# Kernel optimization log

Hardware: AMD Instinct MI355X
Metric: run time of the kernel (lower is better)

## Reference

```python
import jax, jax.numpy as jnp
import numpy as np

B, DIN, DL, DOUT = 8192, 512, 512, 512
L, H, DFF = 6, 8, 2048
E, K = 8, 2
HID = 1024  # int(dim_latent * 2.0)
SLOPE = 0.01
EPS = 1e-5


def _ln(x, s, b):
    m = x.mean(-1, keepdims=True)
    v = ((x - m) ** 2).mean(-1, keepdims=True)
    return (x - m) / jnp.sqrt(v + EPS) * s + b


def _lrelu(x):
    return jnp.where(x >= 0, x, SLOPE * x)


def _mha(q_in, kv_in, in_w, in_b, out_w, out_b):
    # torch nn.MultiheadAttention math (batch_first). in_w: [3d, d]
    d = q_in.shape[-1]
    hd = d // H
    wq, wk, wv = jnp.split(in_w, 3, axis=0)
    bq, bk, bv = jnp.split(in_b, 3, axis=0)
    q = (q_in @ wq.T + bq).reshape(q_in.shape[0], -1, H, hd)
    k = (kv_in @ wk.T + bk).reshape(kv_in.shape[0], -1, H, hd)
    v = (kv_in @ wv.T + bv).reshape(kv_in.shape[0], -1, H, hd)
    scale = jnp.asarray(hd, q.dtype) ** 0.5
    att = jax.nn.softmax(jnp.einsum('bqhd,bkhd->bhqk', q, k) / scale, axis=-1)
    o = jnp.einsum('bhqk,bkhd->bqhd', att, v).reshape(q_in.shape[0], -1, d)
    return o @ out_w.T + out_b


def setup_inputs() -> dict:
    key = jax.random.key(0)
    ks = iter(jax.random.split(key, 64))
    def n(shape, scale=0.02):
        return jax.random.normal(next(ks), shape, dtype=jnp.float32) * scale
    inp = dict(
        src=jax.random.normal(next(ks), (B, 2, DIN), dtype=jnp.float32),
        piw=n((DL, DIN)), pib=n((DL,)), pos=n((1, 2, DL), 1.0),
        ln1_s=jnp.ones((L, DL)), ln1_b=jnp.zeros((L, DL)),
        ln2_s=jnp.ones((L, DL)), ln2_b=jnp.zeros((L, DL)),
        ln3_s=jnp.ones((L, DL)), ln3_b=jnp.zeros((L, DL)),
        sa_in_w=n((L, 3 * DL, DL)), sa_in_b=n((L, 3 * DL)),
        sa_out_w=n((L, DL, DL)), sa_out_b=n((L, DL)),
        ca_in_w=n((L, 3 * DL, DL)), ca_in_b=n((L, 3 * DL)),
        ca_out_w=n((L, DL, DL)), ca_out_b=n((L, DL)),
        ff1_w=n((L, DFF, DL)), ff1_b=n((L, DFF)),
        ff2_w=n((L, DL, DFF)), ff2_b=n((L, DL)),
        r1_w=n((DL // 2, DL)), r1_b=n((DL // 2,)),
        r2_w=n((E, DL // 2)), r2_b=n((E,)),
        se1_w=n((HID, DL)), se1_b=n((HID,)),
        se2_w=n((HID // 2, HID)), se2_b=n((HID // 2,)),
        se3_w=n((DOUT, HID // 2)), se3_b=n((DOUT,)),
        te1_w=n((E, HID, DL)), te1_b=n((E, HID)),
        te2_w=n((E, HID // 2, HID)), te2_b=n((E, HID // 2)),
        te3_w=n((E, DOUT, HID // 2)), te3_b=n((E, DOUT)),
        po_w=n((DOUT, DOUT * (E + 1))), po_b=n((DOUT,)),
    )
    return inp


def reference(src, piw, pib, pos,
              ln1_s, ln1_b, ln2_s, ln2_b, ln3_s, ln3_b,
              sa_in_w, sa_in_b, sa_out_w, sa_out_b,
              ca_in_w, ca_in_b, ca_out_w, ca_out_b,
              ff1_w, ff1_b, ff2_w, ff2_b,
              r1_w, r1_b, r2_w, r2_b,
              se1_w, se1_b, se2_w, se2_b, se3_w, se3_b,
              te1_w, te1_b, te2_w, te2_b, te3_w, te3_b,
              po_w, po_b):
    # input projection + positional encoding; split into tgt (pos 0) / mem (pos 1)
    x = src @ piw.T + pib + pos              # [B, 2, DL]
    tgt, mem = x[:, 0:1], x[:, 1:2]
    # norm_first TransformerDecoderLayer stack (eval: no dropout)
    for i in range(L):
        h = _ln(tgt, ln1_s[i], ln1_b[i])
        tgt = tgt + _mha(h, h, sa_in_w[i], sa_in_b[i], sa_out_w[i], sa_out_b[i])
        h = _ln(tgt, ln2_s[i], ln2_b[i])
        tgt = tgt + _mha(h, mem, ca_in_w[i], ca_in_b[i], ca_out_w[i], ca_out_b[i])
        h = _ln(tgt, ln3_s[i], ln3_b[i])
        tgt = tgt + jax.nn.relu(h @ ff1_w[i].T + ff1_b[i]) @ ff2_w[i].T + ff2_b[i]
    t = tgt[:, 0]                             # [B, DL]
    # shared expert MLP
    sh = _lrelu(t @ se1_w.T + se1_b)
    sh = _lrelu(sh @ se2_w.T + se2_b)
    sh = sh @ se3_w.T + se3_b                 # [B, DOUT]
    # top-k gating (sparse softmax over top-k logits)
    logits = _lrelu(t @ r1_w.T + r1_b) @ r2_w.T + r2_b   # [B, E]
    top_vals, top_idx = jax.lax.top_k(logits, K)
    probs = jax.nn.softmax(top_vals, axis=-1)
    gates = jnp.zeros_like(logits).at[jnp.arange(t.shape[0])[:, None], top_idx].set(probs)
    # dense all-experts compute; non-selected experts get gate=0, which is
    # mathematically identical to the torch mask/gather/scatter dispatch
    h1 = _lrelu(jnp.einsum('bd,ehd->beh', t, te1_w) + te1_b)     # [B,E,HID]
    h2 = _lrelu(jnp.einsum('beh,egh->beg', h1, te2_w) + te2_b)   # [B,E,HID//2]
    eo = jnp.einsum('beg,eog->beo', h2, te3_w) + te3_b           # [B,E,DOUT]
    weighted = (eo * gates[..., None]).reshape(t.shape[0], E * DOUT)
    out = jnp.concatenate([sh, weighted], axis=-1) @ po_w.T + po_b
    return out
```

## Files before the change

### kernel.cpp

```cpp
#include <hip/hip_runtime.h>
#include <hip/hip_bf16.h>

typedef __attribute__((ext_vector_type(8))) short bf8_t;
typedef __attribute__((ext_vector_type(4))) float f4_t;

#define DEV static __device__ __forceinline__

DEV short f2bf(float x){
  unsigned u = __float_as_uint(x);
  u += 0x7fffu + ((u >> 16) & 1u);
  return (short)(u >> 16);
}
DEV float bf2f(short h){
  return __uint_as_float(((unsigned)(unsigned short)h) << 16);
}

DEV void swz(int& bx, int& by){
  int gx = gridDim.x, n = gx * gridDim.y;
  int lb = blockIdx.x + gx * blockIdx.y;
  int q = n >> 3, r = n & 7, xcd = lb & 7, idx = lb >> 3;
  int s = (xcd < r) ? (xcd * (q + 1) + idx) : (r * (q + 1) + (xcd - r) * q + idx);
  bx = s % gx; by = s / gx;
}

template<int TM, int TN, bool SPLIT, int ACT, int MODE, int LB>
__global__ __launch_bounds__(256, LB)
void g2_k(const short* __restrict__ Ahi, const short* __restrict__ Alo, int lda,
          const short* __restrict__ Whi, const short* __restrict__ Wlo, int ldw, long wzs,
          const float* __restrict__ bias, long bzs,
          const float* __restrict__ res, int ldres,
          const float* __restrict__ scale,
          float* __restrict__ Df, int ldd,
          short* __restrict__ Dhi, short* __restrict__ Dlo, int lddp,
          const int* __restrict__ off, const int* __restrict__ perm, int K)
{
  constexpr int NS = SPLIT ? 2 : 1;
  constexpr int TM2 = TM / 2, TN2 = TN / 2, AM = TM / 32, AN = TN / 32;
  constexpr int AIT = TM / 64, BIT = TN / 64;
  __shared__ short As[NS][TM][40];
  __shared__ short Bs[NS][TN][40];

  int bx, by; swz(bx, by);
  const int rowStart = by * TM, colStart = bx * TN;
  if constexpr (MODE >= 1) {
    if (rowStart >= off[8]) return;
    int e = 0;
    while (rowStart >= off[e + 1]) ++e;
    Whi += (long)e * wzs;
    if constexpr (SPLIT) Wlo += (long)e * wzs;
    bias += (long)e * bzs;
  }

  const int tid = threadIdx.x, lane = tid & 63, wid = tid >> 6;
  const int wr = wid >> 1, wc = wid & 1, fr = lane & 15, kg = lane >> 4;

  f4_t acc[AM][AN];
#pragma unroll
  for (int m = 0; m < AM; m++)
#pragma unroll
    for (int n = 0; n < AN; n++)
#pragma unroll
      for (int j = 0; j < 4; j++) acc[m][n][j] = 0.f;

  const short* pAh[AIT]; const short* pAl[AIT]; int aLr[AIT], aLc[AIT];
#pragma unroll
  for (int it = 0; it < AIT; it++) {
    int idx = tid + it * 256, r = idx >> 2, c8 = (idx & 3) << 3;
    aLr[it] = r; aLc[it] = c8;
    long rg = rowStart + r;
    if constexpr (MODE == 2) { int p = perm[rg]; rg = p < 0 ? 0 : p; }
    pAh[it] = Ahi + rg * (long)lda + c8;
    if constexpr (SPLIT) pAl[it] = Alo + rg * (long)lda + c8;
  }
  const short* pBh[BIT]; const short* pBl[BIT]; int bLr[BIT], bLc[BIT];
#pragma unroll
  for (int it = 0; it < BIT; it++) {
    int idx = tid + it * 256, r = idx >> 2, c8 = (idx & 3) << 3;
    bLr[it] = r; bLc[it] = c8;
    long rg = colStart + r;
    pBh[it] = Whi + rg * (long)ldw + c8;
    if constexpr (SPLIT) pBl[it] = Wlo + rg * (long)ldw + c8;
  }

  for (int kb = 0; kb < K; kb += 32) {
    bf8_t va[AIT], val[AIT], vb[BIT], vbl[BIT];
#pragma unroll
    for (int it = 0; it < AIT; it++) {
      va[it] = *(const bf8_t*)(pAh[it] + kb);
      if constexpr (SPLIT) val[it] = *(const bf8_t*)(pAl[it] + kb);
    }
#pragma unroll
    for (int it = 0; it < BIT; it++) {
      vb[it] = *(const bf8_t*)(pBh[it] + kb);
      if constexpr (SPLIT) vbl[it] = *(const bf8_t*)(pBl[it] + kb);
    }
    __syncthreads();
#pragma unroll
    for (int it = 0; it < AIT; it++) {
      *(bf8_t*)&As[0][aLr[it]][aLc[it]] = va[it];
      if constexpr (SPLIT) *(bf8_t*)&As[1][aLr[it]][aLc[it]] = val[it];
    }
#pragma unroll
    for (int it = 0; it < BIT; it++) {
      *(bf8_t*)&Bs[0][bLr[it]][bLc[it]] = vb[it];
      if constexpr (SPLIT) *(bf8_t*)&Bs[1][bLr[it]][bLc[it]] = vbl[it];
    }
    __syncthreads();

    bf8_t a0[AM], a1[AM], b0[AN], b1[AN];
#pragma unroll
    for (int m = 0; m < AM; m++) {
      a0[m] = *(const bf8_t*)&As[0][wr * TM2 + m * 16 + fr][kg * 8];
      if constexpr (SPLIT) a1[m] = *(const bf8_t*)&As[1][wr * TM2 + m * 16 + fr][kg * 8];
    }
#pragma unroll
    for (int n = 0; n < AN; n++) {
      b0[n] = *(const bf8_t*)&Bs[0][wc * TN2 + n * 16 + fr][kg * 8];
      if constexpr (SPLIT) b1[n] = *(const bf8_t*)&Bs[1][wc * TN2 + n * 16 + fr][kg * 8];
    }
#pragma unroll
    for (int m = 0; m < AM; m++)
#pragma unroll
      for (int n = 0; n < AN; n++) {
        acc[m][n] = __builtin_amdgcn_mfma_f32_16x16x32_bf16(a0[m], b0[n], acc[m][n], 0, 0, 0);
        if constexpr (SPLIT) {
          acc[m][n] = __builtin_amdgcn_mfma_f32_16x16x32_bf16(a0[m], b1[n], acc[m][n], 0, 0, 0);
          acc[m][n] = __builtin_amdgcn_mfma_f32_16x16x32_bf16(a1[m], b0[n], acc[m][n], 0, 0, 0);
        }
      }
  }

#pragma unroll
  for (int m = 0; m < AM; m++) {
#pragma unroll
    for (int n = 0; n < AN; n++) {
      const int col = colStart + wc * TN2 + n * 16 + fr;
#pragma unroll
      for (int j = 0; j < 4; j++) {
        const int row = rowStart + wr * TM2 + m * 16 + kg * 4 + j;
        float v = acc[m][n][j];
        if (bias) v += bias[col];
        if (ACT == 1) v = fmaxf(v, 0.f);
        if (ACT == 2) v = (v >= 0.f) ? v : 0.01f * v;
        if (scale) v *= scale[row];
        if (res) v += res[(size_t)row * ldres + col];
        if (Df) Df[(size_t)row * ldd + col] = v;
        if (Dhi) {
          short h = f2bf(v);
          Dhi[(size_t)row * lddp + col] = h;
          if (Dlo) Dlo[(size_t)row * lddp + col] = f2bf(v - bf2f(h));
        }
      }
    }
  }
}

template<bool SPLIT, bool DEMUX>
__global__ __launch_bounds__(256, 2)
void g1_k(const float* __restrict__ A, int lda, long zsA,
          const float* __restrict__ W, int ldw, long zsB,
          const float* __restrict__ bias, int posbias,
          float* __restrict__ Df, short* __restrict__ Dhi, short* __restrict__ Dlo,
          int ldd, long zsD, int K)
{
  constexpr int NS = SPLIT ? 2 : 1;
  __shared__ short As[NS][128][40];
  __shared__ short Bs[NS][128][40];
  const long z = blockIdx.z;
  A += z * zsA; W += z * zsB;
  if (Df)  Df  += z * zsD;
  if (Dhi) Dhi += z * zsD;

  int bx, by; swz(bx, by);
  const int tid = threadIdx.x, lane = tid & 63, wid = tid >> 6;
  const int wr = wid >> 1, wc = wid & 1, fr = lane & 15, kg = lane >> 4;

  f4_t acc[4][4];
#pragma unroll
  for (int m = 0; m < 4; m++)
#pragma unroll
    for (int n = 0; n < 4; n++)
#pragma unroll
      for (int j = 0; j < 4; j++) acc[m][n][j] = 0.f;

  const int srow = tid >> 1, skoff = (tid & 1) << 4;
  const float* pA = A + (size_t)((size_t)by * 128 + srow) * lda + skoff;
  const float* pW = W + (size_t)((size_t)bx * 128 + srow) * ldw + skoff;

  for (int kb = 0; kb < K; kb += 32) {
    float va[16], vw[16];
    {
      const f4_t* a4 = (const f4_t*)(pA + kb);
      const f4_t* w4 = (const f4_t*)(pW + kb);
#pragma unroll
      for (int q = 0; q < 4; q++) {
        f4_t ta = a4[q], tw = w4[q];
#pragma unroll
        for (int j = 0; j < 4; j++) { va[q * 4 + j] = ta[j]; vw[q * 4 + j] = tw[j]; }
      }
    }
    __syncthreads();
#pragma unroll
    for (int h = 0; h < 2; h++) {
      bf8_t ha, hw;
#pragma unroll
      for (int j = 0; j < 8; j++) { ha[j] = f2bf(va[h * 8 + j]); hw[j] = f2bf(vw[h * 8 + j]); }
      *(bf8_t*)&As[0][srow][skoff + h * 8] = ha;
      *(bf8_t*)&Bs[0][srow][skoff + h * 8] = hw;
      if constexpr (SPLIT) {
        bf8_t la, lw;
#pragma unroll
        for (int j = 0; j < 8; j++) {
          la[j] = f2bf(va[h * 8 + j] - bf2f(ha[j]));
          lw[j] = f2bf(vw[h * 8 + j] - bf2f(hw[j]));
        }
        *(bf8_t*)&As[NS - 1][srow][skoff + h * 8] = la;
        *(bf8_t*)&Bs[NS - 1][srow][skoff + h * 8] = lw;
      }
    }
    __syncthreads();

    bf8_t a0[4], b0[4], a1[4], b1[4];
#pragma unroll
    for (int m = 0; m < 4; m++) {
      a0[m] = *(const bf8_t*)&As[0][wr * 64 + m * 16 + fr][kg * 8];
      if constexpr (SPLIT) a1[m] = *(const bf8_t*)&As[NS - 1][wr * 64 + m * 16 + fr][kg * 8];
    }
#pragma unroll
    for (int n = 0; n < 4; n++) {
      b0[n] = *(const bf8_t*)&Bs[0][wc * 64 + n * 16 + fr][kg * 8];
      if constexpr (SPLIT) b1[n] = *(const bf8_t*)&Bs[NS - 1][wc * 64 + n * 16 + fr][kg * 8];
    }
#pragma unroll
    for (int m = 0; m < 4; m++)
#pragma unroll
      for (int n = 0; n < 4; n++) {
        acc[m][n] = __builtin_amdgcn_mfma_f32_16x16x32_bf16(a0[m], b0[n], acc[m][n], 0, 0, 0);
        if constexpr (SPLIT) {
          acc[m][n] = __builtin_amdgcn_mfma_f32_16x16x32_bf16(a0[m], b1[n], acc[m][n], 0, 0, 0);
          acc[m][n] = __builtin_amdgcn_mfma_f32_16x16x32_bf16(a1[m], b0[n], acc[m][n], 0, 0, 0);
        }
      }
  }

  const int Ncols = (int)gridDim.x * 128;
#pragma unroll
  for (int m = 0; m < 4; m++) {
#pragma unroll
    for (int n = 0; n < 4; n++) {
      const int col = bx * 128 + wc * 64 + n * 16 + fr;
#pragma unroll
      for (int j = 0; j < 4; j++) {
        const int row = by * 128 + wr * 64 + m * 16 + kg * 4 + j;
        float v = acc[m][n][j];
        if (bias) v += bias[posbias ? ((row & 1) * Ncols + col) : col];
        if constexpr (DEMUX) {
          const size_t o = (size_t)(row >> 1) * ldd + col;
          if (row & 1) { short h = f2bf(v); Dhi[o] = h; Dlo[o] = f2bf(v - bf2f(h)); }
          else Df[o] = v;
        } else {
          if (Dhi) Dhi[(size_t)row * ldd + col] = f2bf(v);
          else     Df[(size_t)row * ldd + col] = v;
        }
      }
    }
  }
}

__global__ __launch_bounds__(256)
void ln2_k(const float* __restrict__ x, int ldx,
           const float* __restrict__ s, const float* __restrict__ b,
           short* __restrict__ hi, short* __restrict__ lo, int ldy)
{
  const int lane = threadIdx.x & 63;
  const int row = blockIdx.x * 4 + (threadIdx.x >> 6);
  const float* xr = x + (size_t)row * ldx + lane * 8;
  f4_t v0 = *(const f4_t*)xr;
  f4_t v1 = *(const f4_t*)(xr + 4);
  float sum = (v0[0] + v0[1]) + (v0[2] + v0[3]) + ((v1[0] + v1[1]) + (v1[2] + v1[3]));
#pragma unroll
  for (int o = 32; o; o >>= 1) sum += __shfl_xor(sum, o, 64);
  const float mean = sum * (1.f / 512.f);
  float vs = 0.f;
#pragma unroll
  for (int j = 0; j < 4; j++) { float d0 = v0[j] - mean, d1 = v1[j] - mean; vs += d0 * d0 + d1 * d1; }
#pragma unroll
  for (int o = 32; o; o >>= 1) vs += __shfl_xor(vs, o, 64);
  const float rstd = rsqrtf(vs * (1.f / 512.f) + 1e-5f);
  const float* sp = s + lane * 8; const float* bp = b + lane * 8;
  bf8_t h, l;
#pragma unroll
  for (int j = 0; j < 4; j++) {
    float y0 = (v0[j] - mean) * rstd * sp[j] + bp[j];
    float y1 = (v1[j] - mean) * rstd * sp[j + 4] + bp[j + 4];
    short h0 = f2bf(y0); h[j] = h0;     l[j] = f2bf(y0 - bf2f(h0));
    short h1 = f2bf(y1); h[j + 4] = h1; l[j + 4] = f2bf(y1 - bf2f(h1));
  }
  *(bf8_t*)&hi[(size_t)row * ldy + lane * 8] = h;
  *(bf8_t*)&lo[(size_t)row * ldy + lane * 8] = l;
}

__global__ __launch_bounds__(256)
void conv_k(const float* __restrict__ src, long zs, int ld, int cols,
            short* __restrict__ hi, short* __restrict__ lo, long dzs)
{
  const long z = blockIdx.z;
  int idx = blockIdx.x * 256 + threadIdx.x;
  int cpr = cols >> 3;
  int row = idx / cpr, c8 = (idx % cpr) << 3;
  const float* p = src + z * zs + (size_t)row * ld + c8;
  f4_t v0 = *(const f4_t*)p, v1 = *(const f4_t*)(p + 4);
  bf8_t h, l;
#pragma unroll
  for (int j = 0; j < 4; j++) {
    short h0 = f2bf(v0[j]); h[j] = h0;     l[j] = f2bf(v0[j] - bf2f(h0));
    short h1 = f2bf(v1[j]); h[j + 4] = h1; l[j + 4] = f2bf(v1[j] - bf2f(h1));
  }
  size_t dof = (size_t)z * dzs + (size_t)row * cols + c8;
  *(bf8_t*)&hi[dof] = h;
  if (lo) *(bf8_t*)&lo[dof] = l;
}

__global__ __launch_bounds__(256)
void tr_k(const float* __restrict__ in, float* __restrict__ out)
{
  __shared__ float t[32][33];
  const int e = blockIdx.z, ob = blockIdx.x * 32, gb = blockIdx.y * 32;
  const int tx = threadIdx.x & 31, ty = threadIdx.x >> 5;
  const float* I = in + ((size_t)e * 512 + ob) * 512 + gb;
  float* O = out + ((size_t)e * 512 + gb) * 512 + ob;
#pragma unroll
  for (int i = 0; i < 4; i++) t[ty + 8 * i][tx] = I[(size_t)(ty + 8 * i) * 512 + tx];
  __syncthreads();
#pragma unroll
  for (int i = 0; i < 4; i++) O[(size_t)(ty + 8 * i) * 512 + tx] = t[tx][ty + 8 * i];
}

__global__ __launch_bounds__(256)
void bc_k(const float* __restrict__ po, const float* __restrict__ te3b, float* __restrict__ bc)
{
  int idx = blockIdx.x * 256 + threadIdx.x;
  int e = idx >> 9, oo = idx & 511;
  const float* p = po + (size_t)oo * 4608 + 512 + (size_t)e * 512;
  const float* tb = te3b + (size_t)e * 512;
  float s = 0.f;
#pragma unroll 4
  for (int g = 0; g < 512; g += 4) {
    f4_t a = *(const f4_t*)(p + g);
    f4_t b = *(const f4_t*)(tb + g);
    s += a[0] * b[0] + a[1] * b[1] + a[2] * b[2] + a[3] * b[3];
  }
  bc[idx] = s;
}

__global__ __launch_bounds__(256)
void init_k(int* __restrict__ cnt, int* __restrict__ perm, float* __restrict__ pgate)
{
  int i = blockIdx.x * 256 + threadIdx.x;
  if (i < 16) cnt[i] = 0;
  if (i < 17408) { perm[i] = -1; pgate[i] = 0.f; }
}

__global__ __launch_bounds__(256)
void router_k(const float* __restrict__ R1, const float* __restrict__ r2w,
              const float* __restrict__ r2b, int2* __restrict__ ridx,
              float2* __restrict__ rgv, int* __restrict__ cnt)
{
  const int lane = threadIdx.x & 63;
  const int row = blockIdx.x * 4 + (threadIdx.x >> 6);
  f4_t xv = *(const f4_t*)(R1 + (size_t)row * 256 + lane * 4);
  float lg[8];
#pragma unroll
  for (int e = 0; e < 8; e++) {
    f4_t wv = *(const f4_t*)(r2w + e * 256 + lane * 4);
    float p = xv[0] * wv[0] + xv[1] * wv[1] + xv[2] * wv[2] + xv[3] * wv[3];
#pragma unroll
    for (int o = 32; o; o >>= 1) p += __shfl_xor(p, o, 64);
    lg[e] = p + r2b[e];
  }
  int i1 = 0; float v1 = lg[0];
#pragma unroll
  for (int e = 1; e < 8; e++) if (lg[e] > v1) { v1 = lg[e]; i1 = e; }
  int i2 = -1; float v2 = -3.4e38f;
#pragma unroll
  for (int e = 0; e < 8; e++) if (e != i1 && lg[e] > v2) { v2 = lg[e]; i2 = e; }
  const float p2 = 1.f / (1.f + expf(v1 - v2));
  const float p1 = 1.f - p2;
  if (lane == 0) {
    ridx[row] = make_int2(i1, i2);
    rgv[row] = make_float2(p1, p2);
    atomicAdd(&cnt[i1], 1); atomicAdd(&cnt[i2], 1);
  }
}

__global__ void offs_k(const int* __restrict__ cnt, int* __restrict__ off)
{
  if (threadIdx.x == 0) {
    int a = 0; off[0] = 0;
    for (int e = 0; e < 8; e++) { a += (cnt[e] + 127) & ~127; off[e + 1] = a; }
  }
}

__global__ __launch_bounds__(256)
void scat_k(const int2* __restrict__ ridx, const float2* __restrict__ rgv,
            const int* __restrict__ off, int* __restrict__ fill,
            int* __restrict__ perm, float* __restrict__ pgate, int2* __restrict__ islot)
{
  int r = blockIdx.x * 256 + threadIdx.x;
  int2 ii = ridx[r]; float2 gg = rgv[r];
  int p0 = off[ii.x] + atomicAdd(&fill[ii.x], 1); perm[p0] = r; pgate[p0] = gg.x;
  int p1 = off[ii.y] + atomicAdd(&fill[ii.y], 1); perm[p1] = r; pgate[p1] = gg.y;
  islot[r] = make_int2(p0, p1);
}

__global__ __launch_bounds__(256)
void fadd_k(const int2* __restrict__ islot, const float* __restrict__ EO, float* __restrict__ out)
{
  int idx = blockIdx.x * 256 + threadIdx.x;
  int r = idx >> 7, c4 = (idx & 127) << 2;
  int2 s = islot[r];
  f4_t a = *(const f4_t*)&EO[(size_t)s.x * 512 + c4];
  f4_t b = *(const f4_t*)&EO[(size_t)s.y * 512 + c4];
  float* op = &out[(size_t)r * 512 + c4];
  f4_t o = *(const f4_t*)op;
#pragma unroll
  for (int j = 0; j < 4; j++) o[j] += a[j] + b[j];
  *(f4_t*)op = o;
}

__global__ void bias2_k(const float* __restrict__ pib, const float* __restrict__ pos,
                        float* __restrict__ bias2)
{
  int i = blockIdx.x * 256 + threadIdx.x;
  if (i < 1024) bias2[i] = pib[i & 511] + pos[i];
}


extern "C" void kernel_launch(void* const* d_in, const int* in_sizes, int n_in,
                              void* d_out, int out_size, void* d_ws, size_t ws_size,
                              hipStream_t stream)
{
  (void)in_sizes; (void)n_in; (void)out_size; (void)ws_size;
  const float* src     = (const float*)d_in[0];
  const float* piw     = (const float*)d_in[1];
  const float* pib     = (const float*)d_in[2];
  const float* pos     = (const float*)d_in[3];
  const float* ln1_s   = (const float*)d_in[4];
  const float* ln1_b   = (const float*)d_in[5];
  const float* ln3_s   = (const float*)d_in[8];
  const float* ln3_b   = (const float*)d_in[9];
  const float* sa_in_w = (const float*)d_in[10];
  const float* sa_in_b = (const float*)d_in[11];
  const float* sa_ow   = (const float*)d_in[12];
  const float* sa_ob   = (const float*)d_in[13];
  const float* ca_in_w = (const float*)d_in[14];
  const float* ca_in_b = (const float*)d_in[15];
  const float* ca_ow   = (const float*)d_in[16];
  const float* ca_ob   = (const float*)d_in[17];
  const float* ff1_w   = (const float*)d_in[18];
  const float* ff1_b   = (const float*)d_in[19];
  const float* ff2_w   = (const float*)d_in[20];
  const float* ff2_b   = (const float*)d_in[21];
  const float* r1_w    = (const float*)d_in[22];
  const float* r1_b    = (const float*)d_in[23];
  const float* r2_w    = (const float*)d_in[24];
  const float* r2_b    = (const float*)d_in[25];
  const float* se1_w   = (const float*)d_in[26];
  const float* se1_b   = (const float*)d_in[27];
  const float* se2_w   = (const float*)d_in[28];
  const float* se2_b   = (const float*)d_in[29];
  const float* se3_w   = (const float*)d_in[30];
  const float* se3_b   = (const float*)d_in[31];
  const float* te1_w   = (const float*)d_in[32];
  const float* te1_b   = (const float*)d_in[33];
  const float* te2_w   = (const float*)d_in[34];
  const float* te2_b   = (const float*)d_in[35];
  const float* te3_w   = (const float*)d_in[36];
  const float* te3_b   = (const float*)d_in[37];
  const float* po_w    = (const float*)d_in[38];
  const float* po_b    = (const float*)d_in[39];
  float* out = (float*)d_out;

  const size_t MiB = 1048576;
  char* base = (char*)d_ws;
  float* tgt   = (float*)(base + 0 * MiB);
  short* MemHi = (short*)(base + 16 * MiB);
  short* MemLo = (short*)(base + 24 * MiB);
  short* Hhi   = (short*)(base + 32 * MiB);
  short* Hlo   = (short*)(base + 40 * MiB);
  short* Fhi   = (short*)(base + 48 * MiB);
  short* Flo   = (short*)(base + 80 * MiB);
  short* Vhi   = (short*)(base + 48 * MiB);
  short* Vlo   = (short*)(base + 56 * MiB);
  short* wsV   = (short*)(base + 112 * MiB);
  short* saVhi = wsV;             short* saVlo = wsV + 262144;
  short* saOhi = wsV + 524288;    short* saOlo = wsV + 786432;
  short* caVhi = wsV + 1048576;   short* caVlo = wsV + 1310720;
  short* caOhi = wsV + 1572864;   short* caOlo = wsV + 1835008;
  short* ff1hi = (short*)(base + 116 * MiB);  short* ff1lo = ff1hi + 1048576;
  short* ff2hi = (short*)(base + 120 * MiB);  short* ff2lo = ff2hi + 1048576;
  short* tgtHi = Hhi;  short* tgtLo = Hlo;
  float* te3T  = (float*)(base + 0 * MiB);
  short* S1hi  = (short*)(base + 0 * MiB);
  short* S2hi  = (short*)(base + 16 * MiB);
  short* SHhi  = (short*)(base + 24 * MiB);
  short* X1hi  = (short*)(base + 48 * MiB);
  short* X2hi  = (short*)(base + 82 * MiB);
  float* EO    = (float*)(base + 48 * MiB);
  float* F2    = (float*)(base + 104 * MiB);
  short* te1hi = (short*)(base + 104 * MiB);
  short* te2hi = (short*)(base + 112 * MiB);
  short* Wchi  = (short*)(base + 120 * MiB);
  char*  ps    = base + 124 * MiB;
  size_t cur = 0;
  auto alloc = [&](size_t bytes) { char* r = ps + cur; cur = (cur + bytes + 255) & ~(size_t)255; return r; };
  float*  bias2 = (float*)alloc(1024 * 4);
  float*  bc    = (float*)alloc(4096 * 4);
  int*    cnt   = (int*)  alloc(64 * 4);
  int*    fill  = cnt + 8;
  int*    offs  = cnt + 16;
  int2*   ridx  = (int2*) alloc(8192 * 8);
  float2* rgv   = (float2*)alloc(8192 * 8);
  int2*   islot = (int2*) alloc(8192 * 8);
  int*    perm  = (int*)  alloc(17408 * 4);
  float*  pgate = (float*)alloc(17408 * 4);
  short*  r1hi  = (short*)alloc(524288);  short* r1lo = r1hi + 131072;
  short*  se1hi = (short*)alloc(1048576);
  short*  se2hi = (short*)alloc(1048576);
  short*  se3hi = (short*)alloc(524288);
  short*  pomhi = (short*)alloc(524288);

  auto conv = [&](const float* s_, long zs, int ld, int rows, int cols, int z,
                  short* hi, short* lo, long dzs) {
    conv_k<<<dim3(rows * cols / 2048, 1, z), dim3(256), 0, stream>>>(s_, zs, ld, cols, hi, lo, dzs);
  };

  bias2_k<<<dim3(4), dim3(256), 0, stream>>>(pib, pos, bias2);
  conv(r1_w, 0, 512, 256, 512, 1, r1hi, r1lo, 0);
  conv(se1_w, 0, 512, 1024, 512, 1, se1hi, nullptr, 0);
  conv(se2_w, 0, 1024, 512, 1024, 1, se2hi, nullptr, 0);
  conv(se3_w, 0, 512, 512, 512, 1, se3hi, nullptr, 0);
  conv(po_w, 0, 4608, 512, 512, 1, pomhi, nullptr, 0);
  bc_k<<<dim3(16), dim3(256), 0, stream>>>(po_w, te3_b, bc);

  g1_k<true, true><<<dim3(4, 128, 1), dim3(256), 0, stream>>>(
      src, 512, 0, piw, 512, 0, bias2, 1, tgt, MemHi, MemLo, 512, 0, 512);

  for (int i = 0; i < 6; i++) {
    conv(sa_in_w + (size_t)i * 786432 + 524288, 0, 512, 512, 512, 1, saVhi, saVlo, 0);
    conv(sa_ow + (size_t)i * 262144, 0, 512, 512, 512, 1, saOhi, saOlo, 0);
    conv(ca_in_w + (size_t)i * 786432 + 524288, 0, 512, 512, 512, 1, caVhi, caVlo, 0);
    conv(ca_ow + (size_t)i * 262144, 0, 512, 512, 512, 1, caOhi, caOlo, 0);
    conv(ff1_w + (size_t)i * 1048576, 0, 512, 2048, 512, 1, ff1hi, ff1lo, 0);
    conv(ff2_w + (size_t)i * 1048576, 0, 2048, 512, 2048, 1, ff2hi, ff2lo, 0);

    ln2_k<<<dim3(2048), dim3(256), 0, stream>>>(tgt, 512, ln1_s + i * 512, ln1_b + i * 512, Hhi, Hlo, 512);
    g2_k<64, 128, true, 0, 0, 2><<<dim3(4, 128), 256, 0, stream>>>(
        Hhi, Hlo, 512, saVhi, saVlo, 512, 0, sa_in_b + i * 1536 + 1024, 0,
        nullptr, 0, nullptr, nullptr, 0, Vhi, Vlo, 512, nullptr, nullptr, 512);
    g2_k<64, 128, true, 0, 0, 2><<<dim3(4, 128), 256, 0, stream>>>(
        Vhi, Vlo, 512, saOhi, saOlo, 512, 0, sa_ob + i * 512, 0,
        tgt, 512, nullptr, tgt, 512, nullptr, nullptr, 0, nullptr, nullptr, 512);
    g2_k<64, 128, true, 0, 0, 2><<<dim3(4, 128), 256, 0, stream>>>(
        MemHi, MemLo, 512, caVhi, caVlo, 512, 0, ca_in_b + i * 1536 + 1024, 0,
        nullptr, 0, nullptr, nullptr, 0, Vhi, Vlo, 512, nullptr, nullptr, 512);
    g2_k<64, 128, true, 0, 0, 2><<<dim3(4, 128), 256, 0, stream>>>(
        Vhi, Vlo, 512, caOhi, caOlo, 512, 0, ca_ob + i * 512, 0,
        tgt, 512, nullptr, tgt, 512, nullptr, nullptr, 0, nullptr, nullptr, 512);
    ln2_k<<<dim3(2048), dim3(256), 0, stream>>>(tgt, 512, ln3_s + i * 512, ln3_b + i * 512, Hhi, Hlo, 512);
    g2_k<128, 128, true, 1, 0, 2><<<dim3(16, 64), 256, 0, stream>>>(
        Hhi, Hlo, 512, ff1hi, ff1lo, 512, 0, ff1_b + i * 2048, 0,
        nullptr, 0, nullptr, nullptr, 0, Fhi, Flo, 2048, nullptr, nullptr, 512);
    bool last = (i == 5);
    g2_k<64, 128, true, 0, 0, 2><<<dim3(4, 128), 256, 0, stream>>>(
        Fhi, Flo, 2048, ff2hi, ff2lo, 2048, 0, ff2_b + i * 512, 0,
        tgt, 512, nullptr, tgt, 512,
        last ? tgtHi : nullptr, last ? tgtLo : nullptr, 512, nullptr, nullptr, 2048);
  }

  init_k<<<dim3(68), dim3(256), 0, stream>>>(cnt, perm, pgate);
  g2_k<64, 128, true, 2, 0, 2><<<dim3(2, 128), 256, 0, stream>>>(
      tgtHi, tgtLo, 512, r1hi, r1lo, 512, 0, r1_b, 0,
      nullptr, 0, nullptr, F2, 256, nullptr, nullptr, 0, nullptr, nullptr, 512);
  router_k<<<dim3(2048), dim3(256), 0, stream>>>(F2, r2_w, r2_b, ridx, rgv, cnt);
  offs_k<<<dim3(1), dim3(64), 0, stream>>>(cnt, offs);
  scat_k<<<dim3(32), dim3(256), 0, stream>>>(ridx, rgv, offs, fill, perm, pgate, islot);

  tr_k<<<dim3(16, 16, 8), dim3(256), 0, stream>>>(te3_w, te3T);
  g1_k<false, false><<<dim3(4, 4, 8), dim3(256), 0, stream>>>(
      po_w + 512, 4608, 512, te3T, 512, 262144,
      nullptr, 0, nullptr, Wchi, nullptr, 512, 262144, 512);
  conv(te1_w, 524288, 512, 1024, 512, 8, te1hi, nullptr, 524288);
  conv(te2_w, 524288, 1024, 512, 1024, 8, te2hi, nullptr, 524288);

  g2_k<128, 128, false, 2, 0, 3><<<dim3(8, 64), 256, 0, stream>>>(
      tgtHi, nullptr, 512, se1hi, nullptr, 512, 0, se1_b, 0,
      nullptr, 0, nullptr, nullptr, 0, S1hi, nullptr, 1024, nullptr, nullptr, 512);
  g2_k<64, 128, false, 2, 0, 4><<<dim3(4, 128), 256, 0, stream>>>(
      S1hi, nullptr, 1024, se2hi, nullptr, 1024, 0, se2_b, 0,
      nullptr, 0, nullptr, nullptr, 0, S2hi, nullptr, 512, nullptr, nullptr, 1024);
  g2_k<64, 128, false, 0, 0, 4><<<dim3(4, 128), 256, 0, stream>>>(
      S2hi, nullptr, 512, se3hi, nullptr, 512, 0, se3_b, 0,
      nullptr, 0, nullptr, nullptr, 0, SHhi, nullptr, 512, nullptr, nullptr, 512);
  g2_k<64, 128, false, 0, 0, 4><<<dim3(4, 128), 256, 0, stream>>>(
      SHhi, nullptr, 512, pomhi, nullptr, 512, 0, po_b, 0,
      nullptr, 0, nullptr, out, 512, nullptr, nullptr, 0, nullptr, nullptr, 512);

  g2_k<128, 128, false, 2, 2, 3><<<dim3(8, 136), 256, 0, stream>>>(
      tgtHi, nullptr, 512, te1hi, nullptr, 512, 524288, te1_b, 1024,
      nullptr, 0, nullptr, nullptr, 0, X1hi, nullptr, 1024, offs, perm, 512);
  g2_k<64, 128, false, 2, 1, 4><<<dim3(4, 272), 256, 0, stream>>>(
      X1hi, nullptr, 1024, te2hi, nullptr, 1024, 524288, te2_b, 512,
      nullptr, 0, nullptr, nullptr, 0, X2hi, nullptr, 512, offs, nullptr, 1024);
  g2_k<64, 128, false, 0, 1, 4><<<dim3(4, 272), 256, 0, stream>>>(
      X2hi, nullptr, 512, Wchi, nullptr, 512, 262144, bc, 512,
      nullptr, 0, pgate, EO, 512, nullptr, nullptr, 0, offs, nullptr, 512);
  fadd_k<<<dim3(4096), dim3(256), 0, stream>>>(islot, EO, out);
}
```

Baseline: 2.822 ms.

## Fuse MoE dispatch into one ballot-based kernel and retune GEMM template parameter

Replaces the init, atomic-count, offset and atomic-scatter kernels with a single 1024-thread block. It counts experts per wave with ballots, builds the offsets in shared memory and assigns slots deterministically. This removes three launches and the global atomics. Separately, the last template parameter of most transformer-layer GEMMs changes from 2 to 4 (3 for ff1), which likely alters occupancy or pipelining depth. The single-block scheduler serialises 8192 rows on one CU, which adds some latency.

```diff
diff --git a/kernel.cpp b/kernel.cpp
--- a/kernel.cpp
+++ b/kernel.cpp
@@ -354,17 +354,9 @@
 }
 
 __global__ __launch_bounds__(256)
-void init_k(int* __restrict__ cnt, int* __restrict__ perm, float* __restrict__ pgate)
-{
-  int i = blockIdx.x * 256 + threadIdx.x;
-  if (i < 16) cnt[i] = 0;
-  if (i < 17408) { perm[i] = -1; pgate[i] = 0.f; }
-}
-
-__global__ __launch_bounds__(256)
 void router_k(const float* __restrict__ R1, const float* __restrict__ r2w,
               const float* __restrict__ r2b, int2* __restrict__ ridx,
-              float2* __restrict__ rgv, int* __restrict__ cnt)
+              float2* __restrict__ rgv)
 {
   const int lane = threadIdx.x & 63;
   const int row = blockIdx.x * 4 + (threadIdx.x >> 6);
@@ -389,28 +381,76 @@
   if (lane == 0) {
     ridx[row] = make_int2(i1, i2);
     rgv[row] = make_float2(p1, p2);
-    atomicAdd(&cnt[i1], 1); atomicAdd(&cnt[i2], 1);
-  }
-}
-
-__global__ void offs_k(const int* __restrict__ cnt, int* __restrict__ off)
-{
-  if (threadIdx.x == 0) {
-    int a = 0; off[0] = 0;
-    for (int e = 0; e < 8; e++) { a += (cnt[e] + 127) & ~127; off[e + 1] = a; }
-  }
-}
-
-__global__ __launch_bounds__(256)
-void scat_k(const int2* __restrict__ ridx, const float2* __restrict__ rgv,
-            const int* __restrict__ off, int* __restrict__ fill,
-            int* __restrict__ perm, float* __restrict__ pgate, int2* __restrict__ islot)
-{
-  int r = blockIdx.x * 256 + threadIdx.x;
-  int2 ii = ridx[r]; float2 gg = rgv[r];
-  int p0 = off[ii.x] + atomicAdd(&fill[ii.x], 1); perm[p0] = r; pgate[p0] = gg.x;
-  int p1 = off[ii.y] + atomicAdd(&fill[ii.y], 1); perm[p1] = r; pgate[p1] = gg.y;
-  islot[r] = make_int2(p0, p1);
+  }
+}
+
+__global__ __launch_bounds__(1024, 1)
+void sched_k(const int2* __restrict__ ridx, const float2* __restrict__ rgv,
+             int* __restrict__ offs, int* __restrict__ perm,
+             float* __restrict__ pgate, int2* __restrict__ islot)
+{
+  __shared__ int wcnt[16][8];
+  __shared__ int wbase[16][8];
+  __shared__ int soff[9];
+  const int tid = threadIdx.x, lane = tid & 63, w = tid >> 6;
+  const unsigned long long below = (lane == 63) ? 0x7FFFFFFFFFFFFFFFULL
+                                                : ((1ULL << lane) - 1);
+  int2 rid[8]; float2 rgl[8];
+  int cnt[8];
+#pragma unroll
+  for (int e = 0; e < 8; e++) cnt[e] = 0;
+#pragma unroll
+  for (int it = 0; it < 8; it++) {
+    int r = w * 512 + it * 64 + lane;
+    rid[it] = ridx[r]; rgl[it] = rgv[r];
+#pragma unroll
+    for (int e = 0; e < 8; e++) {
+      unsigned long long m0 = __ballot(rid[it].x == e);
+      unsigned long long m1 = __ballot(rid[it].y == e);
+      cnt[e] += (int)__popcll(m0) + (int)__popcll(m1);
+    }
+  }
+  if (lane == 0) {
+#pragma unroll
+    for (int e = 0; e < 8; e++) wcnt[w][e] = cnt[e];
+  }
+  __syncthreads();
+  if (tid == 0) {
+    int a = 0; soff[0] = 0;
+    for (int e = 0; e < 8; e++) {
+      int run = a, tot = 0;
+      for (int ww = 0; ww < 16; ww++) { wbase[ww][e] = run; run += wcnt[ww][e]; tot += wcnt[ww][e]; }
+      a += (tot + 127) & ~127;
+      soff[e + 1] = a;
+    }
+  }
+  __syncthreads();
+  if (tid < 9) offs[tid] = soff[tid];
+  for (int i = tid; i < 17408; i += 1024) { perm[i] = -1; pgate[i] = 0.f; }
+  __syncthreads();
+  int cur[8];
+#pragma unroll
+  for (int e = 0; e < 8; e++) cur[e] = wbase[w][e];
+#pragma unroll
+  for (int it = 0; it < 8; it++) {
+    int r = w * 512 + it * 64 + lane;
+    int p0 = 0, p1 = 0;
+#pragma unroll
+    for (int e = 0; e < 8; e++) {
+      unsigned long long m = __ballot(rid[it].x == e);
+      if (rid[it].x == e) p0 = cur[e] + (int)__popcll(m & below);
+      cur[e] += (int)__popcll(m);
+    }
+#pragma unroll
+    for (int e = 0; e < 8; e++) {
+      unsigned long long m = __ballot(rid[it].y == e);
+      if (rid[it].y == e) p1 = cur[e] + (int)__popcll(m & below);
+      cur[e] += (int)__popcll(m);
+    }
+    perm[p0] = r; pgate[p0] = rgl[it].x;
+    perm[p1] = r; pgate[p1] = rgl[it].y;
+    islot[r] = make_int2(p0, p1);
+  }
 }
 
 __global__ __launch_bounds__(256)
@@ -516,9 +556,7 @@
   auto alloc = [&](size_t bytes) { char* r = ps + cur; cur = (cur + bytes + 255) & ~(size_t)255; return r; };
   float*  bias2 = (float*)alloc(1024 * 4);
   float*  bc    = (float*)alloc(4096 * 4);
-  int*    cnt   = (int*)  alloc(64 * 4);
-  int*    fill  = cnt + 8;
-  int*    offs  = cnt + 16;
+  int*    offs  = (int*)  alloc(64 * 4);
   int2*   ridx  = (int2*) alloc(8192 * 8);
   float2* rgv   = (float2*)alloc(8192 * 8);
   int2*   islot = (int2*) alloc(8192 * 8);
@@ -555,36 +593,34 @@
     conv(ff2_w + (size_t)i * 1048576, 0, 2048, 512, 2048, 1, ff2hi, ff2lo, 0);
 
     ln2_k<<<dim3(2048), dim3(256), 0, stream>>>(tgt, 512, ln1_s + i * 512, ln1_b + i * 512, Hhi, Hlo, 512);
-    g2_k<64, 128, true, 0, 0, 2><<<dim3(4, 128), 256, 0, stream>>>(
+    g2_k<64, 128, true, 0, 0, 4><<<dim3(4, 128), 256, 0, stream>>>(
         Hhi, Hlo, 512, saVhi, saVlo, 512, 0, sa_in_b + i * 1536 + 1024, 0,
         nullptr, 0, nullptr, nullptr, 0, Vhi, Vlo, 512, nullptr, nullptr, 512);
-    g2_k<64, 128, true, 0, 0, 2><<<dim3(4, 128), 256, 0, stream>>>(
+    g2_k<64, 128, true, 0, 0, 4><<<dim3(4, 128), 256, 0, stream>>>(
         Vhi, Vlo, 512, saOhi, saOlo, 512, 0, sa_ob + i * 512, 0,
         tgt, 512, nullptr, tgt, 512, nullptr, nullptr, 0, nullptr, nullptr, 512);
-    g2_k<64, 128, true, 0, 0, 2><<<dim3(4, 128), 256, 0, stream>>>(
+    g2_k<64, 128, true, 0, 0, 4><<<dim3(4, 128), 256, 0, stream>>>(
         MemHi, MemLo, 512, caVhi, caVlo, 512, 0, ca_in_b + i * 1536 + 1024, 0,
         nullptr, 0, nullptr, nullptr, 0, Vhi, Vlo, 512, nullptr, nullptr, 512);
-    g2_k<64, 128, true, 0, 0, 2><<<dim3(4, 128), 256, 0, stream>>>(
+    g2_k<64, 128, true, 0, 0, 4><<<dim3(4, 128), 256, 0, stream>>>(
         Vhi, Vlo, 512, caOhi, caOlo, 512, 0, ca_ob + i * 512, 0,
         tgt, 512, nullptr, tgt, 512, nullptr, nullptr, 0, nullptr, nullptr, 512);
     ln2_k<<<dim3(2048), dim3(256), 0, stream>>>(tgt, 512, ln3_s + i * 512, ln3_b + i * 512, Hhi, Hlo, 512);
-    g2_k<128, 128, true, 1, 0, 2><<<dim3(16, 64), 256, 0, stream>>>(
+    g2_k<128, 128, true, 1, 0, 3><<<dim3(16, 64), 256, 0, stream>>>(
         Hhi, Hlo, 512, ff1hi, ff1lo, 512, 0, ff1_b + i * 2048, 0,
         nullptr, 0, nullptr, nullptr, 0, Fhi, Flo, 2048, nullptr, nullptr, 512);
     bool last = (i == 5);
-    g2_k<64, 128, true, 0, 0, 2><<<dim3(4, 128), 256, 0, stream>>>(
+    g2_k<64, 128, true, 0, 0, 4><<<dim3(4, 128), 256, 0, stream>>>(
         Fhi, Flo, 2048, ff2hi, ff2lo, 2048, 0, ff2_b + i * 512, 0,
         tgt, 512, nullptr, tgt, 512,
         last ? tgtHi : nullptr, last ? tgtLo : nullptr, 512, nullptr, nullptr, 2048);
   }
 
-  init_k<<<dim3(68), dim3(256), 0, stream>>>(cnt, perm, pgate);
-  g2_k<64, 128, true, 2, 0, 2><<<dim3(2, 128), 256, 0, stream>>>(
+  g2_k<64, 128, true, 2, 0, 4><<<dim3(2, 128), 256, 0, stream>>>(
       tgtHi, tgtLo, 512, r1hi, r1lo, 512, 0, r1_b, 0,
       nullptr, 0, nullptr, F2, 256, nullptr, nullptr, 0, nullptr, nullptr, 512);
-  router_k<<<dim3(2048), dim3(256), 0, stream>>>(F2, r2_w, r2_b, ridx, rgv, cnt);
-  offs_k<<<dim3(1), dim3(64), 0, stream>>>(cnt, offs);
-  scat_k<<<dim3(32), dim3(256), 0, stream>>>(ridx, rgv, offs, fill, perm, pgate, islot);
+  router_k<<<dim3(2048), dim3(256), 0, stream>>>(F2, r2_w, r2_b, ridx, rgv);
+  sched_k<<<dim3(1), dim3(1024), 0, stream>>>(ridx, rgv, offs, perm, pgate, islot);
 
   tr_k<<<dim3(16, 16, 8), dim3(256), 0, stream>>>(te3_w, te3T);
   g1_k<false, false><<<dim3(4, 4, 8), dim3(256), 0, stream>>>(
```

Result: faster. 2.513 ms (-11.0%).
